# Optimization experiments

Hardware: AMD Instinct MI355X
Metric: run time of the kernel (lower is better)

Reference implementation:

```python
import jax, jax.numpy as jnp
import numpy as np


def _rms_norm(x, g, eps=1e-6):
    # WanRMSNorm over the full channel dim
    return x * jax.lax.rsqrt(jnp.mean(x * x, axis=-1, keepdims=True) + eps) * g


def _rope_apply(x, angles, f, h, w, start_frame):
    # x: [B, L, n, d]; angles: [1024, d//2] (real rotation angles; torch version
    # stores exp(i*theta) complex and multiplies in float64 -- same rotation math).
    B, L, n, d = x.shape
    c = d // 2
    c1 = c // 3
    c0 = c - 2 * c1  # band split [22, 21, 21] for c=64
    af = angles[start_frame:start_frame + f, :c0]        # [f, c0]
    ah = angles[:h, c0:c0 + c1]                          # [h, c1]
    aw = angles[:w, c0 + c1:]                            # [w, c1]
    ang = jnp.concatenate([
        jnp.broadcast_to(af[:, None, None, :], (f, h, w, c0)),
        jnp.broadcast_to(ah[None, :, None, :], (f, h, w, c1)),
        jnp.broadcast_to(aw[None, None, :, :], (f, h, w, c1)),
    ], axis=-1).reshape(1, L, 1, c)
    cos, sin = jnp.cos(ang), jnp.sin(ang)
    xr = x.reshape(B, L, n, c, 2)
    re, im = xr[..., 0], xr[..., 1]  # consecutive-pair complex layout
    out = jnp.stack([re * cos - im * sin, re * sin + im * cos], axis=-1)
    return out.reshape(B, L, n, d)


def reference(x, freqs, Wq, bq, Wk, bk, Wv, bv, Wo, bo, gq, gk,
              f, h, w, num_heads, local_attn_size, sink_size, start_frame):
    B, L, dim = x.shape
    n = num_heads
    d = dim // n
    # QKV projections + RMSNorm on q,k over full dim (as in the module)
    q = _rms_norm(x @ Wq.T + bq, gq).reshape(B, L, n, d)
    k = _rms_norm(x @ Wk.T + bk, gk).reshape(B, L, n, d)
    v = (x @ Wv.T + bv).reshape(B, L, n, d)
    rq = _rope_apply(q, freqs, f, h, w, start_frame)
    rk = _rope_apply(k, freqs, f, h, w, start_frame)
    # frame-level causal + local window + sink mask (the flex_attention block_mask)
    frame_idx = jnp.arange(L) // (h * w)
    fi, fj = frame_idx[:, None], frame_idx[None, :]
    mask = (fj <= fi) & ((fi - fj < local_attn_size) | (fj < sink_size))  # [L, L]
    scores = jnp.einsum('bqhd,bkhd->bhqk', rq, rk) / np.float32(np.sqrt(d))
    scores = jnp.where(mask, scores, -jnp.inf)
    p = jax.nn.softmax(scores, axis=-1)
    out = jnp.einsum('bhqk,bkhd->bqhd', p, v).reshape(B, L, dim)
    return out @ Wo.T + bo


def setup_inputs() -> dict:
    key = jax.random.key(0)
    dim, num_heads = 1536, 12
    f, h, w = 3, 30, 52
    L = f * h * w  # 4680
    d = dim // num_heads  # 128
    c = d // 2  # 64
    ks = jax.random.split(key, 6)
    scale = 0.02
    def lin(k):
        return jax.random.normal(k, (dim, dim), jnp.float32) * scale
    x = jax.random.normal(ks[0], (1, L, dim), jnp.float32)
    inv = 1.0 / (10000.0 ** (np.arange(c, dtype=np.float64) / c))
    freqs = jnp.asarray(np.outer(np.arange(1024), inv), jnp.float32)
    return {
        'x': x, 'freqs': freqs,
        'Wq': lin(ks[1]), 'bq': jnp.zeros(dim, jnp.float32),
        'Wk': lin(ks[2]), 'bk': jnp.zeros(dim, jnp.float32),
        'Wv': lin(ks[3]), 'bv': jnp.zeros(dim, jnp.float32),
        'Wo': lin(ks[4]), 'bo': jnp.zeros(dim, jnp.float32),
        'gq': jnp.ones(dim, jnp.float32), 'gk': jnp.ones(dim, jnp.float32),
        'f': f, 'h': h, 'w': w, 'num_heads': num_heads,
        'local_attn_size': 3, 'sink_size': 1, 'start_frame': 0,
    }
```

## Files before the change

kernel.cpp:

```cpp
#include <hip/hip_runtime.h>
#include <hip/hip_bf16.h>
#include <math.h>

typedef __bf16 bf16_t;
typedef __attribute__((ext_vector_type(8))) __bf16 bf16x8;
typedef __attribute__((ext_vector_type(4))) __bf16 bf16x4;
typedef __attribute__((ext_vector_type(4))) float f32x4;

#define L_TOK 4680
#define DIM   1536
#define NH    12
#define HD    128
#define FRAME 1560
#define LPAD  4736
#define SCALE 0.08838834764831845f

__device__ __forceinline__ void gl_lds16(const bf16_t* g, bf16_t* l) {
  __builtin_amdgcn_global_load_lds(
      (const __attribute__((address_space(1))) unsigned int*)(g),
      (__attribute__((address_space(3))) unsigned int*)(l),
      16, 0, 0);
}

__global__ __launch_bounds__(256) void cast_f32_bf16(const float* __restrict__ in,
                                                     bf16_t* __restrict__ out, int n4) {
  int i = blockIdx.x * 256 + threadIdx.x;
  if (i >= n4) return;
  float4 v = ((const float4*)in)[i];
  bf16x4 o;
  o[0] = (__bf16)v.x; o[1] = (__bf16)v.y; o[2] = (__bf16)v.z; o[3] = (__bf16)v.w;
  ((bf16x4*)out)[i] = o;
}

__global__ __launch_bounds__(256) void gemm_qkv(
    const bf16_t* __restrict__ X,
    const bf16_t* __restrict__ Wq, const bf16_t* __restrict__ Wk, const bf16_t* __restrict__ Wv,
    const float* __restrict__ bq, const float* __restrict__ bk, const float* __restrict__ bv,
    bf16_t* __restrict__ Qo, bf16_t* __restrict__ Ko, bf16_t* __restrict__ Vt)
{
  __shared__ __align__(16) bf16_t Al[128 * 32];
  __shared__ __align__(16) bf16_t Bl[128 * 32];
  const int m0 = blockIdx.x * 128;
  const int nb = blockIdx.y;
  const int seg = nb / 12;
  const int n0 = (nb % 12) * 128;
  const bf16_t* W   = (seg == 0) ? Wq : (seg == 1) ? Wk : Wv;
  const float* bias = (seg == 0) ? bq : (seg == 1) ? bk : bv;

  const int tid = threadIdx.x;
  const int wave = tid >> 6, lane = tid & 63;
  const int quad = lane >> 4, l15 = lane & 15;
  const int wm = (wave >> 1) * 64, wn = (wave & 1) * 64;

  f32x4 acc[4][4];
#pragma unroll
  for (int i = 0; i < 4; ++i)
#pragma unroll
    for (int j = 0; j < 4; ++j) acc[i][j] = (f32x4){0.f, 0.f, 0.f, 0.f};

  const int c0 = wave * 2;
  const int fi0 = c0 * 512 + lane * 8;
  const int r0 = fi0 >> 5, col0 = fi0 & 31;
  const int fi1 = fi0 + 512;
  const int r1 = fi1 >> 5, col1 = fi1 & 31;

  const bf16_t* agp0 = X + (size_t)(m0 + r0) * DIM + col0;
  const bf16_t* agp1 = X + (size_t)(m0 + r1) * DIM + col1;
  const bf16_t* bgp0 = W + (size_t)(n0 + r0) * DIM + col0;
  const bf16_t* bgp1 = W + (size_t)(n0 + r1) * DIM + col1;
  bf16_t* al0 = Al + c0 * 512 + lane * 8;
  bf16_t* al1 = al0 + 512;
  bf16_t* bl0 = Bl + c0 * 512 + lane * 8;
  bf16_t* bl1 = bl0 + 512;

  for (int k0 = 0; k0 < DIM; k0 += 32) {
    __syncthreads();
    gl_lds16(agp0 + k0, al0);
    gl_lds16(agp1 + k0, al1);
    gl_lds16(bgp0 + k0, bl0);
    gl_lds16(bgp1 + k0, bl1);
    __syncthreads();
    bf16x8 af[4], bfg[4];
#pragma unroll
    for (int i = 0; i < 4; ++i) {
      af[i]  = *(const bf16x8*)(Al + (wm + i * 16 + l15) * 32 + quad * 8);
      bfg[i] = *(const bf16x8*)(Bl + (wn + i * 16 + l15) * 32 + quad * 8);
    }
#pragma unroll
    for (int i = 0; i < 4; ++i)
#pragma unroll
      for (int j = 0; j < 4; ++j)
        acc[i][j] = __builtin_amdgcn_mfma_f32_16x16x32_bf16(af[i], bfg[j], acc[i][j], 0, 0, 0);
  }

  if (seg < 2) {
    bf16_t* Out = (seg == 0) ? Qo : Ko;
#pragma unroll
    for (int i = 0; i < 4; ++i) {
#pragma unroll
      for (int j = 0; j < 4; ++j) {
        const int n = n0 + wn + j * 16 + l15;
        const float bb = bias[n];
#pragma unroll
        for (int r = 0; r < 4; ++r) {
          const int m = m0 + wm + i * 16 + quad * 4 + r;
          if (m < L_TOK) Out[(size_t)m * DIM + n] = (bf16_t)(acc[i][j][r] + bb);
        }
      }
    }
  } else {
#pragma unroll
    for (int i = 0; i < 4; ++i) {
      const int mb = m0 + wm + i * 16 + quad * 4;
      if (mb < L_TOK) {
#pragma unroll
        for (int j = 0; j < 4; ++j) {
          const int n = n0 + wn + j * 16 + l15;
          const float bb = bias[n];
          bf16x4 p;
          p[0] = (__bf16)(acc[i][j][0] + bb);
          p[1] = (__bf16)(acc[i][j][1] + bb);
          p[2] = (__bf16)(acc[i][j][2] + bb);
          p[3] = (__bf16)(acc[i][j][3] + bb);
          *(bf16x4*)(Vt + (size_t)n * LPAD + mb) = p;
        }
      }
    }
  }
}

__global__ __launch_bounds__(256) void rmsnorm_rope(
    bf16_t* __restrict__ Q, bf16_t* __restrict__ K,
    const float* __restrict__ gq, const float* __restrict__ gk,
    const float* __restrict__ freqs)
{
  const int l = blockIdx.x;
  const int tid = threadIdx.x;
  const int wave = tid >> 6, lane = tid & 63;
  bf16_t* qrow = Q + (size_t)l * DIM;
  bf16_t* krow = K + (size_t)l * DIM;

  unsigned int qb[3], kb[3];
  float sq = 0.f, sk = 0.f;
#pragma unroll
  for (int s = 0; s < 3; ++s) {
    const int p = s * 256 + tid;
    qb[s] = *(const unsigned int*)(qrow + 2 * p);
    kb[s] = *(const unsigned int*)(krow + 2 * p);
    const __bf16* qh = (const __bf16*)&qb[s];
    const __bf16* kh = (const __bf16*)&kb[s];
    const float q0 = (float)qh[0], q1 = (float)qh[1];
    const float k0 = (float)kh[0], k1 = (float)kh[1];
    sq += q0 * q0 + q1 * q1;
    sk += k0 * k0 + k1 * k1;
  }
#pragma unroll
  for (int off = 1; off < 64; off <<= 1) {
    sq += __shfl_xor(sq, off);
    sk += __shfl_xor(sk, off);
  }
  __shared__ float rq_s[4], rk_s[4];
  if (lane == 0) { rq_s[wave] = sq; rk_s[wave] = sk; }
  __syncthreads();
  sq = rq_s[0] + rq_s[1] + rq_s[2] + rq_s[3];
  sk = rk_s[0] + rk_s[1] + rk_s[2] + rk_s[3];
  const float rnq = rsqrtf(sq * (1.f / DIM) + 1e-6f);
  const float rnk = rsqrtf(sk * (1.f / DIM) + 1e-6f);

  const int t = l / FRAME;
  const int rem = l - t * FRAME;
  const int hh = rem / 52;
  const int ww = rem - hh * 52;

#pragma unroll
  for (int s = 0; s < 3; ++s) {
    const int p = s * 256 + tid;
    const int j = p & 63;
    const int sel = (j < 22) ? t : (j < 43) ? hh : ww;
    const float ang = freqs[sel * 64 + j];
    float sn, cs;
    __sincosf(ang, &sn, &cs);
    const __bf16* qh = (const __bf16*)&qb[s];
    const __bf16* kh = (const __bf16*)&kb[s];
    {
      const float g0 = gq[2 * p], g1 = gq[2 * p + 1];
      const float re = (float)qh[0] * rnq * g0;
      const float im = (float)qh[1] * rnq * g1;
      unsigned int o;
      __bf16* oh = (__bf16*)&o;
      oh[0] = (__bf16)((re * cs - im * sn) * SCALE);
      oh[1] = (__bf16)((re * sn + im * cs) * SCALE);
      *(unsigned int*)(qrow + 2 * p) = o;
    }
    {
      const float g0 = gk[2 * p], g1 = gk[2 * p + 1];
      const float re = (float)kh[0] * rnk * g0;
      const float im = (float)kh[1] * rnk * g1;
      unsigned int o;
      __bf16* oh = (__bf16*)&o;
      oh[0] = (__bf16)(re * cs - im * sn);
      oh[1] = (__bf16)(re * sn + im * cs);
      *(unsigned int*)(krow + 2 * p) = o;
    }
  }
}

__global__ __launch_bounds__(256) void attn(
    const bf16_t* __restrict__ Q, const bf16_t* __restrict__ K,
    const bf16_t* __restrict__ Vt, bf16_t* __restrict__ O)
{
  __shared__ __align__(16) bf16_t Kl[64][136];
  __shared__ __align__(16) bf16_t Vl[128][72];
  __shared__ __align__(16) float  Sl[4][16][68];

  const int qb = (int)gridDim.x - 1 - (int)blockIdx.x;
  const int h = blockIdx.y;
  const int tid = threadIdx.x;
  const int wave = tid >> 6, lane = tid & 63;
  const int quad = lane >> 4, l15 = lane & 15;
  const int q0 = qb * 64;

  bf16x8 qf[4];
  {
    const int qrow = q0 + wave * 16 + l15;
    const bf16_t* qp = Q + (size_t)qrow * DIM + h * HD + quad * 8;
#pragma unroll
    for (int s = 0; s < 4; ++s) qf[s] = *(const bf16x8*)(qp + s * 32);
  }
  const int rr = lane >> 2, part = lane & 3;
  const int myl = q0 + wave * 16 + rr;
  const int lcl = (myl < L_TOK - 1) ? myl : (L_TOK - 1);
  const int kend = FRAME * (lcl / FRAME + 1);
  float m_run = -__builtin_inff(), l_run = 0.f;
  f32x4 oacc[8];
#pragma unroll
  for (int i = 0; i < 8; ++i) oacc[i] = (f32x4){0.f, 0.f, 0.f, 0.f};

  const int lastl = (q0 + 63 < L_TOK - 1) ? (q0 + 63) : (L_TOK - 1);
  const int nkt = (FRAME * (lastl / FRAME + 1) + 63) >> 6;

  for (int kt = 0; kt < nkt; ++kt) {
    const int kb = kt * 64;
    __syncthreads();
#pragma unroll
    for (int it = 0; it < 4; ++it) {
      const int c = tid + it * 256;
      const int r = c >> 4, cc = (c & 15) << 3;
      *(uint4*)(&Kl[r][cc]) = *(const uint4*)(K + (size_t)(kb + r) * DIM + h * HD + cc);
    }
#pragma unroll
    for (int it = 0; it < 4; ++it) {
      const int c = tid + it * 256;
      const int d = c >> 3, cc = (c & 7) << 3;
      *(uint4*)(&Vl[d][cc]) = *(const uint4*)(Vt + (size_t)(h * HD + d) * LPAD + kb + cc);
    }
    __syncthreads();

    f32x4 s[4];
#pragma unroll
    for (int nt = 0; nt < 4; ++nt) s[nt] = (f32x4){0.f, 0.f, 0.f, 0.f};
#pragma unroll
    for (int ds = 0; ds < 4; ++ds) {
#pragma unroll
      for (int nt = 0; nt < 4; ++nt) {
        bf16x8 kf = *(const bf16x8*)(&Kl[nt * 16 + l15][ds * 32 + quad * 8]);
        s[nt] = __builtin_amdgcn_mfma_f32_16x16x32_bf16(qf[ds], kf, s[nt], 0, 0, 0);
      }
    }
#pragma unroll
    for (int nt = 0; nt < 4; ++nt)
#pragma unroll
      for (int r = 0; r < 4; ++r)
        Sl[wave][quad * 4 + r][nt * 16 + l15] = s[nt][r];
    __builtin_amdgcn_wave_barrier();

    float vals[16];
    float mx = -__builtin_inff();
#pragma unroll
    for (int c4 = 0; c4 < 4; ++c4) {
      float4 v = *(const float4*)(&Sl[wave][rr][part * 16 + c4 * 4]);
      const float* vv = (const float*)&v;
#pragma unroll
      for (int jj = 0; jj < 4; ++jj) {
        const int col = kb + part * 16 + c4 * 4 + jj;
        const float sv = (col < kend) ? vv[jj] : -__builtin_inff();
        vals[c4 * 4 + jj] = sv;
        mx = fmaxf(mx, sv);
      }
    }
    mx = fmaxf(mx, __shfl_xor(mx, 1));
    mx = fmaxf(mx, __shfl_xor(mx, 2));
    const float m_new = fmaxf(m_run, mx);
    float ssum = 0.f;
#pragma unroll
    for (int c4 = 0; c4 < 4; ++c4) {
      float4 pv;
      float* pp = (float*)&pv;
#pragma unroll
      for (int jj = 0; jj < 4; ++jj) {
        const float p = __expf(vals[c4 * 4 + jj] - m_new);
        pp[jj] = p;
        ssum += p;
      }
      *(float4*)(&Sl[wave][rr][part * 16 + c4 * 4]) = pv;
    }
    __builtin_amdgcn_wave_barrier();
    ssum += __shfl_xor(ssum, 1);
    ssum += __shfl_xor(ssum, 2);
    const float alpha = __expf(m_run - m_new);
    l_run = l_run * alpha + ssum;
    m_run = m_new;

    const float a0 = __shfl(alpha, (quad * 4 + 0) * 4);
    const float a1 = __shfl(alpha, (quad * 4 + 1) * 4);
    const float a2 = __shfl(alpha, (quad * 4 + 2) * 4);
    const float a3 = __shfl(alpha, (quad * 4 + 3) * 4);
#pragma unroll
    for (int nt = 0; nt < 8; ++nt) {
      oacc[nt][0] *= a0; oacc[nt][1] *= a1; oacc[nt][2] *= a2; oacc[nt][3] *= a3;
    }

    bf16x8 pf[2];
#pragma unroll
    for (int kk = 0; kk < 2; ++kk) {
      float4 f0 = *(const float4*)(&Sl[wave][l15][kk * 32 + quad * 8]);
      float4 f1 = *(const float4*)(&Sl[wave][l15][kk * 32 + quad * 8 + 4]);
      bf16x8 t;
      t[0] = (__bf16)f0.x; t[1] = (__bf16)f0.y; t[2] = (__bf16)f0.z; t[3] = (__bf16)f0.w;
      t[4] = (__bf16)f1.x; t[5] = (__bf16)f1.y; t[6] = (__bf16)f1.z; t[7] = (__bf16)f1.w;
      pf[kk] = t;
    }
#pragma unroll
    for (int nt = 0; nt < 8; ++nt) {
#pragma unroll
      for (int kk = 0; kk < 2; ++kk) {
        bf16x8 vf = *(const bf16x8*)(&Vl[nt * 16 + l15][kk * 32 + quad * 8]);
        oacc[nt] = __builtin_amdgcn_mfma_f32_16x16x32_bf16(pf[kk], vf, oacc[nt], 0, 0, 0);
      }
    }
  }

  const float li = 1.f / l_run;
  const float li0 = __shfl(li, (quad * 4 + 0) * 4);
  const float li1 = __shfl(li, (quad * 4 + 1) * 4);
  const float li2 = __shfl(li, (quad * 4 + 2) * 4);
  const float li3 = __shfl(li, (quad * 4 + 3) * 4);
  const int mrow = q0 + wave * 16 + quad * 4;
  if (mrow < L_TOK) {
#pragma unroll
    for (int nt = 0; nt < 8; ++nt) {
      const int n = h * HD + nt * 16 + l15;
      O[(size_t)(mrow + 0) * DIM + n] = (bf16_t)(oacc[nt][0] * li0);
      O[(size_t)(mrow + 1) * DIM + n] = (bf16_t)(oacc[nt][1] * li1);
      O[(size_t)(mrow + 2) * DIM + n] = (bf16_t)(oacc[nt][2] * li2);
      O[(size_t)(mrow + 3) * DIM + n] = (bf16_t)(oacc[nt][3] * li3);
    }
  }
}

__global__ __launch_bounds__(256) void gemm_proj(
    const bf16_t* __restrict__ A, const bf16_t* __restrict__ W,
    const float* __restrict__ bias, float* __restrict__ out)
{
  __shared__ __align__(16) bf16_t Al[128 * 32];
  __shared__ __align__(16) bf16_t Bl[128 * 32];
  const int m0 = blockIdx.x * 128;
  const int n0 = blockIdx.y * 128;

  const int tid = threadIdx.x;
  const int wave = tid >> 6, lane = tid & 63;
  const int quad = lane >> 4, l15 = lane & 15;
  const int wm = (wave >> 1) * 64, wn = (wave & 1) * 64;

  f32x4 acc[4][4];
#pragma unroll
  for (int i = 0; i < 4; ++i)
#pragma unroll
    for (int j = 0; j < 4; ++j) acc[i][j] = (f32x4){0.f, 0.f, 0.f, 0.f};

  const int c0 = wave * 2;
  const int fi0 = c0 * 512 + lane * 8;
  const int r0 = fi0 >> 5, col0 = fi0 & 31;
  const int fi1 = fi0 + 512;
  const int r1 = fi1 >> 5, col1 = fi1 & 31;

  const bf16_t* agp0 = A + (size_t)(m0 + r0) * DIM + col0;
  const bf16_t* agp1 = A + (size_t)(m0 + r1) * DIM + col1;
  const bf16_t* bgp0 = W + (size_t)(n0 + r0) * DIM + col0;
  const bf16_t* bgp1 = W + (size_t)(n0 + r1) * DIM + col1;
  bf16_t* al0 = Al + c0 * 512 + lane * 8;
  bf16_t* al1 = al0 + 512;
  bf16_t* bl0 = Bl + c0 * 512 + lane * 8;
  bf16_t* bl1 = bl0 + 512;

  for (int k0 = 0; k0 < DIM; k0 += 32) {
    __syncthreads();
    gl_lds16(agp0 + k0, al0);
    gl_lds16(agp1 + k0, al1);
    gl_lds16(bgp0 + k0, bl0);
    gl_lds16(bgp1 + k0, bl1);
    __syncthreads();
    bf16x8 af[4], bfg[4];
#pragma unroll
    for (int i = 0; i < 4; ++i) {
      af[i]  = *(const bf16x8*)(Al + (wm + i * 16 + l15) * 32 + quad * 8);
      bfg[i] = *(const bf16x8*)(Bl + (wn + i * 16 + l15) * 32 + quad * 8);
    }
#pragma unroll
    for (int i = 0; i < 4; ++i)
#pragma unroll
      for (int j = 0; j < 4; ++j)
        acc[i][j] = __builtin_amdgcn_mfma_f32_16x16x32_bf16(af[i], bfg[j], acc[i][j], 0, 0, 0);
  }

#pragma unroll
  for (int i = 0; i < 4; ++i) {
#pragma unroll
    for (int j = 0; j < 4; ++j) {
      const int n = n0 + wn + j * 16 + l15;
      const float bb = bias[n];
#pragma unroll
      for (int r = 0; r < 4; ++r) {
        const int m = m0 + wm + i * 16 + quad * 4 + r;
        if (m < L_TOK) out[(size_t)m * DIM + n] = acc[i][j][r] + bb;
      }
    }
  }
}

extern "C" void kernel_launch(void* const* d_in, const int* in_sizes, int n_in,
                              void* d_out, int out_size, void* d_ws, size_t ws_size,
                              hipStream_t stream) {
  (void)in_sizes; (void)n_in; (void)out_size;
  const float* x  = (const float*)d_in[0];
  const float* fr = (const float*)d_in[1];
  const float* Wq = (const float*)d_in[2];
  const float* bq = (const float*)d_in[3];
  const float* Wk = (const float*)d_in[4];
  const float* bk = (const float*)d_in[5];
  const float* Wv = (const float*)d_in[6];
  const float* bv = (const float*)d_in[7];
  const float* Wo = (const float*)d_in[8];
  const float* bo = (const float*)d_in[9];
  const float* gq = (const float*)d_in[10];
  const float* gk = (const float*)d_in[11];
  float* out = (float*)d_out;

  char* ws = (char*)d_ws;
  size_t off = 0;
  auto alloc = [&](size_t bytes) {
    char* p = ws + off;
    off += (bytes + 255) & ~(size_t)255;
    return p;
  };
  const size_t lbuf = (size_t)LPAD * DIM * 2;
  const size_t wbuf = (size_t)DIM * DIM * 2;
  bf16_t* xb  = (bf16_t*)alloc(lbuf);
  bf16_t* Wqb = (bf16_t*)alloc(wbuf);
  bf16_t* Wkb = (bf16_t*)alloc(wbuf);
  bf16_t* Wvb = (bf16_t*)alloc(wbuf);
  bf16_t* Wob = (bf16_t*)alloc(wbuf);
  bf16_t* Qb  = (bf16_t*)alloc(lbuf);
  bf16_t* Kb  = (bf16_t*)alloc(lbuf);
  bf16_t* Vtb = (bf16_t*)alloc(lbuf);
  bf16_t* Ob  = (bf16_t*)alloc(lbuf);
  if (off > ws_size) return;

  const int n4x = L_TOK * DIM / 4;
  const int n4w = DIM * DIM / 4;
  cast_f32_bf16<<<(n4x + 255) / 256, 256, 0, stream>>>(x, xb, n4x);
  cast_f32_bf16<<<(n4w + 255) / 256, 256, 0, stream>>>(Wq, Wqb, n4w);
  cast_f32_bf16<<<(n4w + 255) / 256, 256, 0, stream>>>(Wk, Wkb, n4w);
  cast_f32_bf16<<<(n4w + 255) / 256, 256, 0, stream>>>(Wv, Wvb, n4w);
  cast_f32_bf16<<<(n4w + 255) / 256, 256, 0, stream>>>(Wo, Wob, n4w);

  gemm_qkv<<<dim3(LPAD / 128, 36), 256, 0, stream>>>(xb, Wqb, Wkb, Wvb, bq, bk, bv,
                                                     Qb, Kb, Vtb);
  rmsnorm_rope<<<L_TOK, 256, 0, stream>>>(Qb, Kb, gq, gk, fr);
  attn<<<dim3(LPAD / 64, NH), 256, 0, stream>>>(Qb, Kb, Vtb, Ob);
  gemm_proj<<<dim3(LPAD / 128, 12), 256, 0, stream>>>(Ob, Wob, bo, out);
}
```

Before: 650.5 us.

## Restructure attention: 128-row Q tiles, register softmax, swizzled LDS, MFMA row-sum

Each block now covers 128 query rows, with every wave handling two 16-row MFMA tiles, so each K/V tile loaded into LDS is reused across twice as many queries. Softmax runs directly on the MFMA accumulators using cross-lane shuffles, which removes the fp32 score round-trip through LDS. P is written to LDS as bf16, and K/V are stored with an XOR swizzle instead of padding to avoid bank conflicts. The row sum comes from an extra ones-row appended to V, and global loads are issued before the barrier. In exchange, register pressure rises sharply (two sets of 9 accumulators) and there are half as many blocks, which may hurt occupancy and load balance.

```diff
diff --git a/kernel.cpp b/kernel.cpp
--- a/kernel.cpp
+++ b/kernel.cpp
@@ -209,151 +209,189 @@
     const bf16_t* __restrict__ Q, const bf16_t* __restrict__ K,
     const bf16_t* __restrict__ Vt, bf16_t* __restrict__ O)
 {
-  __shared__ __align__(16) bf16_t Kl[64][136];
-  __shared__ __align__(16) bf16_t Vl[128][72];
-  __shared__ __align__(16) float  Sl[4][16][68];
+  __shared__ __align__(16) bf16_t Kl[64 * 128];
+  __shared__ __align__(16) bf16_t Vl[144 * 64];
+  __shared__ __align__(16) bf16_t Pl[4][32 * 72];
 
   const int qb = (int)gridDim.x - 1 - (int)blockIdx.x;
-  const int h = blockIdx.y;
+  const int h  = blockIdx.y;
   const int tid = threadIdx.x;
   const int wave = tid >> 6, lane = tid & 63;
   const int quad = lane >> 4, l15 = lane & 15;
-  const int q0 = qb * 64;
-
-  bf16x8 qf[4];
+  const int q0 = qb * 128;
+  const int qw = q0 + wave * 32;
+
   {
-    const int qrow = q0 + wave * 16 + l15;
+    const int r = tid >> 4, c4 = (tid & 15) * 4;
+    const bf16_t v = (r == 0) ? (bf16_t)1.0f : (bf16_t)0.0f;
+    bf16x4 vv = {v, v, v, v};
+    *(bf16x4*)(Vl + (128 + r) * 64 + c4) = vv;
+  }
+
+  bf16x8 qf[2][4];
+#pragma unroll
+  for (int mt = 0; mt < 2; ++mt) {
+    const int qrow = qw + mt * 16 + l15;
     const bf16_t* qp = Q + (size_t)qrow * DIM + h * HD + quad * 8;
 #pragma unroll
-    for (int s = 0; s < 4; ++s) qf[s] = *(const bf16x8*)(qp + s * 32);
-  }
-  const int rr = lane >> 2, part = lane & 3;
-  const int myl = q0 + wave * 16 + rr;
-  const int lcl = (myl < L_TOK - 1) ? myl : (L_TOK - 1);
-  const int kend = FRAME * (lcl / FRAME + 1);
-  float m_run = -__builtin_inff(), l_run = 0.f;
-  f32x4 oacc[8];
-#pragma unroll
-  for (int i = 0; i < 8; ++i) oacc[i] = (f32x4){0.f, 0.f, 0.f, 0.f};
-
-  const int lastl = (q0 + 63 < L_TOK - 1) ? (q0 + 63) : (L_TOK - 1);
+    for (int ds = 0; ds < 4; ++ds) qf[mt][ds] = *(const bf16x8*)(qp + ds * 32);
+  }
+
+  int kendv[2][4];
+#pragma unroll
+  for (int mt = 0; mt < 2; ++mt)
+#pragma unroll
+    for (int r = 0; r < 4; ++r) {
+      int row = qw + mt * 16 + quad * 4 + r;
+      if (row > L_TOK - 1) row = L_TOK - 1;
+      kendv[mt][r] = FRAME * (row / FRAME + 1);
+    }
+  const int kend_blk = FRAME * (q0 / FRAME + 1);
+
+  f32x4 m_run[2], oacc[2][9];
+#pragma unroll
+  for (int mt = 0; mt < 2; ++mt) {
+    m_run[mt] = (f32x4){-3.0e38f, -3.0e38f, -3.0e38f, -3.0e38f};
+#pragma unroll
+    for (int nt = 0; nt < 9; ++nt) oacc[mt][nt] = (f32x4){0.f, 0.f, 0.f, 0.f};
+  }
+
+  int lastl = q0 + 127; if (lastl > L_TOK - 1) lastl = L_TOK - 1;
   const int nkt = (FRAME * (lastl / FRAME + 1) + 63) >> 6;
 
   for (int kt = 0; kt < nkt; ++kt) {
     const int kb = kt * 64;
-    __syncthreads();
+
+    uint4 ku[4], vu[4];
 #pragma unroll
     for (int it = 0; it < 4; ++it) {
       const int c = tid + it * 256;
-      const int r = c >> 4, cc = (c & 15) << 3;
-      *(uint4*)(&Kl[r][cc]) = *(const uint4*)(K + (size_t)(kb + r) * DIM + h * HD + cc);
-    }
+      const int r = c >> 4, cc = c & 15;
+      ku[it] = *(const uint4*)(K + (size_t)(kb + r) * DIM + h * HD + cc * 8);
+      const int d = c >> 3, c8 = c & 7;
+      vu[it] = *(const uint4*)(Vt + (size_t)(h * HD + d) * LPAD + kb + c8 * 8);
+    }
+    __syncthreads();
 #pragma unroll
     for (int it = 0; it < 4; ++it) {
       const int c = tid + it * 256;
-      const int d = c >> 3, cc = (c & 7) << 3;
-      *(uint4*)(&Vl[d][cc]) = *(const uint4*)(Vt + (size_t)(h * HD + d) * LPAD + kb + cc);
+      const int r = c >> 4, cc = c & 15;
+      *(uint4*)(Kl + r * 128 + ((cc ^ (r & 7)) * 8)) = ku[it];
+      const int d = c >> 3, c8 = c & 7;
+      *(uint4*)(Vl + d * 64 + ((c8 ^ (d & 7)) * 8)) = vu[it];
     }
     __syncthreads();
 
-    f32x4 s[4];
-#pragma unroll
-    for (int nt = 0; nt < 4; ++nt) s[nt] = (f32x4){0.f, 0.f, 0.f, 0.f};
+    f32x4 s[2][4];
+#pragma unroll
+    for (int mt = 0; mt < 2; ++mt)
+#pragma unroll
+      for (int nt = 0; nt < 4; ++nt) s[mt][nt] = (f32x4){0.f, 0.f, 0.f, 0.f};
 #pragma unroll
     for (int ds = 0; ds < 4; ++ds) {
 #pragma unroll
       for (int nt = 0; nt < 4; ++nt) {
-        bf16x8 kf = *(const bf16x8*)(&Kl[nt * 16 + l15][ds * 32 + quad * 8]);
-        s[nt] = __builtin_amdgcn_mfma_f32_16x16x32_bf16(qf[ds], kf, s[nt], 0, 0, 0);
-      }
-    }
-#pragma unroll
-    for (int nt = 0; nt < 4; ++nt)
+        const int row = nt * 16 + l15;
+        bf16x8 kf = *(const bf16x8*)(Kl + row * 128 + (((ds * 4 + quad) ^ (l15 & 7)) * 8));
+        s[0][nt] = __builtin_amdgcn_mfma_f32_16x16x32_bf16(qf[0][ds], kf, s[0][nt], 0, 0, 0);
+        s[1][nt] = __builtin_amdgcn_mfma_f32_16x16x32_bf16(qf[1][ds], kf, s[1][nt], 0, 0, 0);
+      }
+    }
+
+    if (kb + 64 > kend_blk) {
+#pragma unroll
+      for (int mt = 0; mt < 2; ++mt)
+#pragma unroll
+        for (int nt = 0; nt < 4; ++nt) {
+          const int col = kb + nt * 16 + l15;
+#pragma unroll
+          for (int r = 0; r < 4; ++r)
+            if (col >= kendv[mt][r]) s[mt][nt][r] = -3.0e38f;
+        }
+    }
+
+    f32x4 alpha[2];
+    int need_resc = 0;
+#pragma unroll
+    for (int mt = 0; mt < 2; ++mt) {
+      f32x4 mx;
 #pragma unroll
       for (int r = 0; r < 4; ++r)
-        Sl[wave][quad * 4 + r][nt * 16 + l15] = s[nt][r];
+        mx[r] = fmaxf(fmaxf(s[mt][0][r], s[mt][1][r]), fmaxf(s[mt][2][r], s[mt][3][r]));
+#pragma unroll
+      for (int r = 0; r < 4; ++r) {
+        float v = mx[r];
+        v = fmaxf(v, __shfl_xor(v, 1));
+        v = fmaxf(v, __shfl_xor(v, 2));
+        v = fmaxf(v, __shfl_xor(v, 4));
+        v = fmaxf(v, __shfl_xor(v, 8));
+        mx[r] = v;
+      }
+#pragma unroll
+      for (int r = 0; r < 4; ++r) {
+        const float m_new = fmaxf(m_run[mt][r], mx[r]);
+        alpha[mt][r] = __expf(m_run[mt][r] - m_new);
+        m_run[mt][r] = m_new;
+        need_resc |= (alpha[mt][r] != 1.0f);
+      }
+    }
+    if (__any(need_resc)) {
+#pragma unroll
+      for (int mt = 0; mt < 2; ++mt)
+#pragma unroll
+        for (int nt = 0; nt < 9; ++nt)
+#pragma unroll
+          for (int r = 0; r < 4; ++r) oacc[mt][nt][r] *= alpha[mt][r];
+    }
+
+#pragma unroll
+    for (int mt = 0; mt < 2; ++mt)
+#pragma unroll
+      for (int nt = 0; nt < 4; ++nt)
+#pragma unroll
+        for (int r = 0; r < 4; ++r) {
+          const float p = __expf(s[mt][nt][r] - m_run[mt][r]);
+          Pl[wave][(mt * 16 + quad * 4 + r) * 72 + nt * 16 + l15] = (bf16_t)p;
+        }
     __builtin_amdgcn_wave_barrier();
 
-    float vals[16];
-    float mx = -__builtin_inff();
-#pragma unroll
-    for (int c4 = 0; c4 < 4; ++c4) {
-      float4 v = *(const float4*)(&Sl[wave][rr][part * 16 + c4 * 4]);
-      const float* vv = (const float*)&v;
-#pragma unroll
-      for (int jj = 0; jj < 4; ++jj) {
-        const int col = kb + part * 16 + c4 * 4 + jj;
-        const float sv = (col < kend) ? vv[jj] : -__builtin_inff();
-        vals[c4 * 4 + jj] = sv;
-        mx = fmaxf(mx, sv);
-      }
-    }
-    mx = fmaxf(mx, __shfl_xor(mx, 1));
-    mx = fmaxf(mx, __shfl_xor(mx, 2));
-    const float m_new = fmaxf(m_run, mx);
-    float ssum = 0.f;
-#pragma unroll
-    for (int c4 = 0; c4 < 4; ++c4) {
-      float4 pv;
-      float* pp = (float*)&pv;
-#pragma unroll
-      for (int jj = 0; jj < 4; ++jj) {
-        const float p = __expf(vals[c4 * 4 + jj] - m_new);
-        pp[jj] = p;
-        ssum += p;
-      }
-      *(float4*)(&Sl[wave][rr][part * 16 + c4 * 4]) = pv;
-    }
-    __builtin_amdgcn_wave_barrier();
-    ssum += __shfl_xor(ssum, 1);
-    ssum += __shfl_xor(ssum, 2);
-    const float alpha = __expf(m_run - m_new);
-    l_run = l_run * alpha + ssum;
-    m_run = m_new;
-
-    const float a0 = __shfl(alpha, (quad * 4 + 0) * 4);
-    const float a1 = __shfl(alpha, (quad * 4 + 1) * 4);
-    const float a2 = __shfl(alpha, (quad * 4 + 2) * 4);
-    const float a3 = __shfl(alpha, (quad * 4 + 3) * 4);
-#pragma unroll
-    for (int nt = 0; nt < 8; ++nt) {
-      oacc[nt][0] *= a0; oacc[nt][1] *= a1; oacc[nt][2] *= a2; oacc[nt][3] *= a3;
-    }
-
-    bf16x8 pf[2];
+    bf16x8 pf[2][2];
+#pragma unroll
+    for (int mt = 0; mt < 2; ++mt)
+#pragma unroll
+      for (int kk = 0; kk < 2; ++kk)
+        pf[mt][kk] = *(const bf16x8*)(&Pl[wave][(mt * 16 + l15) * 72 + kk * 32 + quad * 8]);
 #pragma unroll
     for (int kk = 0; kk < 2; ++kk) {
-      float4 f0 = *(const float4*)(&Sl[wave][l15][kk * 32 + quad * 8]);
-      float4 f1 = *(const float4*)(&Sl[wave][l15][kk * 32 + quad * 8 + 4]);
-      bf16x8 t;
-      t[0] = (__bf16)f0.x; t[1] = (__bf16)f0.y; t[2] = (__bf16)f0.z; t[3] = (__bf16)f0.w;
-      t[4] = (__bf16)f1.x; t[5] = (__bf16)f1.y; t[6] = (__bf16)f1.z; t[7] = (__bf16)f1.w;
-      pf[kk] = t;
-    }
-#pragma unroll
-    for (int nt = 0; nt < 8; ++nt) {
-#pragma unroll
-      for (int kk = 0; kk < 2; ++kk) {
-        bf16x8 vf = *(const bf16x8*)(&Vl[nt * 16 + l15][kk * 32 + quad * 8]);
-        oacc[nt] = __builtin_amdgcn_mfma_f32_16x16x32_bf16(pf[kk], vf, oacc[nt], 0, 0, 0);
-      }
-    }
-  }
-
-  const float li = 1.f / l_run;
-  const float li0 = __shfl(li, (quad * 4 + 0) * 4);
-  const float li1 = __shfl(li, (quad * 4 + 1) * 4);
-  const float li2 = __shfl(li, (quad * 4 + 2) * 4);
-  const float li3 = __shfl(li, (quad * 4 + 3) * 4);
-  const int mrow = q0 + wave * 16 + quad * 4;
-  if (mrow < L_TOK) {
+#pragma unroll
+      for (int nt = 0; nt < 9; ++nt) {
+        const int row = nt * 16 + l15;
+        bf16x8 vf = *(const bf16x8*)(Vl + row * 64 + (((kk * 4 + quad) ^ (l15 & 7)) * 8));
+        oacc[0][nt] = __builtin_amdgcn_mfma_f32_16x16x32_bf16(pf[0][kk], vf, oacc[0][nt], 0, 0, 0);
+        oacc[1][nt] = __builtin_amdgcn_mfma_f32_16x16x32_bf16(pf[1][kk], vf, oacc[1][nt], 0, 0, 0);
+      }
+    }
+  }
+
+  float li[2][4];
+#pragma unroll
+  for (int mt = 0; mt < 2; ++mt)
+#pragma unroll
+    for (int r = 0; r < 4; ++r) {
+      const float lv = __shfl(oacc[mt][8][r], lane & 48);
+      li[mt][r] = 1.0f / lv;
+    }
+#pragma unroll
+  for (int mt = 0; mt < 2; ++mt) {
 #pragma unroll
     for (int nt = 0; nt < 8; ++nt) {
       const int n = h * HD + nt * 16 + l15;
-      O[(size_t)(mrow + 0) * DIM + n] = (bf16_t)(oacc[nt][0] * li0);
-      O[(size_t)(mrow + 1) * DIM + n] = (bf16_t)(oacc[nt][1] * li1);
-      O[(size_t)(mrow + 2) * DIM + n] = (bf16_t)(oacc[nt][2] * li2);
-      O[(size_t)(mrow + 3) * DIM + n] = (bf16_t)(oacc[nt][3] * li3);
+#pragma unroll
+      for (int r = 0; r < 4; ++r) {
+        const int row = qw + mt * 16 + quad * 4 + r;
+        if (row < L_TOK)
+          O[(size_t)row * DIM + n] = (bf16_t)(oacc[mt][nt][r] * li[mt][r]);
+      }
     }
   }
 }
@@ -477,6 +515,6 @@
   gemm_qkv<<<dim3(LPAD / 128, 36), 256, 0, stream>>>(xb, Wqb, Wkb, Wvb, bq, bk, bv,
                                                      Qb, Kb, Vtb);
   rmsnorm_rope<<<L_TOK, 256, 0, stream>>>(Qb, Kb, gq, gk, fr);
-  attn<<<dim3(LPAD / 64, NH), 256, 0, stream>>>(Qb, Kb, Vtb, Ob);
+  attn<<<dim3(LPAD / 128, NH), 256, 0, stream>>>(Qb, Kb, Vtb, Ob);
   gemm_proj<<<dim3(LPAD / 128, 12), 256, 0, stream>>>(Ob, Wob, bo, out);
 }
```

Result: slower. 941.0 us (+44.6%).
